# Performance work log

Measured on AMD Instinct MI355X. Metric: run time of the kernel, lower is better.

The kernel has to match this reference:

```python
import jax, jax.numpy as jnp
import numpy as np

M_MODES = 12
N_PHOTONS = 6  # input_state = [1]*6 + [0]*6


def _glynn_signs(n):
    # All delta in {+1,-1}^n with delta_0 = +1 : 2^(n-1) sign vectors.
    k = np.arange(2 ** (n - 1))
    bits = (k[:, None] >> np.arange(n - 1)[None, :]) & 1  # [S, n-1]
    signs = np.concatenate([np.ones((k.size, 1)), 1.0 - 2.0 * bits], axis=1)
    parity = np.prod(signs, axis=1)  # [S]
    return jnp.asarray(signs, jnp.float32), jnp.asarray(parity, jnp.float32)


def _batched_permanent(Msub):
    # Glynn formula: perm(M) = 2^(1-n) * sum_delta prod(delta) * prod_j sum_i delta_i M_ij
    n = Msub.shape[-1]
    signs, parity = _glynn_signs(n)
    signs = signs.astype(Msub.dtype)
    # [..., S, n] row-sums under each sign vector
    rowsums = jnp.einsum('sn,...nj->...sj', signs, Msub)
    prods = jnp.prod(rowsums, axis=-1)  # [..., S]
    perm = jnp.einsum('s,...s->...', parity.astype(Msub.dtype), prods)
    return perm / (2.0 ** (n - 1))


def _feature_unitaries(x, A, B):
    # U(x) = A @ diag(exp(i x)) @ B  (phase-shifter layer between fixed interferometers)
    ph = jnp.exp(1j * x.astype(jnp.complex64))  # [N, m]
    return jnp.einsum('ab,nb,bc->nac', A, ph, B)  # [N, m, m]


def setup_inputs() -> dict:
    key = jax.random.key(0)
    k1, k2, k3, k4 = jax.random.split(key, 4)
    x1 = jax.random.normal(k1, (384, M_MODES), jnp.float32)
    x2 = jax.random.normal(k2, (384, M_MODES), jnp.float32)
    # Fixed Haar-random unitaries for the interferometer meshes
    rng = np.random.default_rng(0)
    A = np.linalg.qr(rng.normal(size=(M_MODES, M_MODES)) + 1j * rng.normal(size=(M_MODES, M_MODES)))[0]
    B = np.linalg.qr(rng.normal(size=(M_MODES, M_MODES)) + 1j * rng.normal(size=(M_MODES, M_MODES)))[0]
    return {
        'x1': x1, 'x2': x2,
        'A_re': jnp.asarray(A.real, jnp.float32), 'A_im': jnp.asarray(A.imag, jnp.float32),
        'B_re': jnp.asarray(B.real, jnp.float32), 'B_im': jnp.asarray(B.imag, jnp.float32),
    }


def reference(x1, x2, A_re, A_im, B_re, B_im):
    A = (A_re + 1j * A_im).astype(jnp.complex64)
    B = (B_re + 1j * B_im).astype(jnp.complex64)
    U1 = _feature_unitaries(x1, A, B)  # [N1, m, m]
    U2 = _feature_unitaries(x2, A, B)  # [N2, m, m]
    n = N_PHOTONS
    # W = U(x2)^dag U(x1); amplitude = perm(W[s_idx, s_idx]) with s_idx = first n modes
    # (input_state = [1]*n + [0]*(m-n), all factorials = 1)
    Wsub = jnp.einsum('jka,ikb->ijab', jnp.conj(U2[:, :, :n]), U1[:, :, :n])  # [N1,N2,n,n]
    amp = _batched_permanent(Wsub)  # [N1, N2] complex
    K = jnp.abs(amp) ** 2
    return K.astype(jnp.float32)
```

## Files before the change

### kernel.cpp

```cpp
#include <hip/hip_runtime.h>


#define NS 384
#define MM 12
#define NP 6
#define TS 16
#define SV_STRIDE 148

struct c32 { float x, y; };

__device__ __forceinline__ c32 cmul(c32 a, c32 b) {
    c32 r;
    r.x = a.x * b.x - a.y * b.y;
    r.y = a.x * b.y + a.y * b.x;
    return r;
}

__global__ void build_V_kernel(const float* __restrict__ x1,
                               const float* __restrict__ x2,
                               const float* __restrict__ Ar, const float* __restrict__ Ai,
                               const float* __restrict__ Br, const float* __restrict__ Bi,
                               float* __restrict__ V1, float* __restrict__ V2c) {
    int idx = blockIdx.x * blockDim.x + threadIdx.x;
    if (idx >= 2 * NS * NP) return;
    int half = idx / (NS * NP);
    int rem  = idx - half * (NS * NP);
    int s = rem / NP, c = rem - s * NP;
    const float* x = half ? x2 : x1;

    float tr[MM], ti[MM];
#pragma unroll
    for (int b = 0; b < MM; ++b) {
        float sv, cv;
        sincosf(x[s * MM + b], &sv, &cv);
        float br = Br[b * MM + c], bi = Bi[b * MM + c];
        tr[b] = cv * br - sv * bi;
        ti[b] = cv * bi + sv * br;
    }

    float* V = half ? V2c : V1;
    float sgn = half ? -1.f : 1.f;
#pragma unroll
    for (int a = 0; a < MM; ++a) {
        float ure = 0.f, uim = 0.f;
#pragma unroll
        for (int b = 0; b < MM; ++b) {
            float ar = Ar[a * MM + b], ai = Ai[a * MM + b];
            ure = fmaf(ar, tr[b], fmaf(-ai, ti[b], ure));
            uim = fmaf(ar, ti[b], fmaf( ai, tr[b], uim));
        }
        int off = ((s * MM + a) * NP + c) * 2;
        V[off]     = ure;
        V[off + 1] = sgn * uim;
    }
}

__global__ __launch_bounds__(256) void perm_kernel(const float* __restrict__ V1g,
                                                   const float* __restrict__ V2g,
                                                   float* __restrict__ out) {
    __shared__ __align__(16) float sV1[TS * SV_STRIDE];
    __shared__ __align__(16) float sV2[TS * SV_STRIDE];
    const int i0 = blockIdx.y * TS;
    const int j0 = blockIdx.x * TS;
    const int tid = threadIdx.x;

    for (int idx = tid; idx < 2 * TS * 36; idx += 256) {
        int which = idx >= TS * 36;
        int rem = which ? idx - TS * 36 : idx;
        int s = rem / 36, q = rem - s * 36;
        const float* src = which ? (V2g + (j0 + s) * 144) : (V1g + (i0 + s) * 144);
        float4 v = *(const float4*)(src + q * 4);
        float* dst = (which ? sV2 : sV1) + s * SV_STRIDE + q * 4;
        *(float4*)dst = v;
    }
    __syncthreads();

    const int tx = tid & 15, ty = tid >> 4;
    const float* v1 = sV1 + ty * SV_STRIDE;
    const float* v2 = sV2 + tx * SV_STRIDE;

    c32 W[NP][NP];
#pragma unroll
    for (int a = 0; a < NP; ++a)
#pragma unroll
        for (int b = 0; b < NP; ++b) { W[a][b].x = 0.f; W[a][b].y = 0.f; }

#pragma unroll
    for (int k = 0; k < MM; ++k) {
        float4 p1[3], p2[3];
#pragma unroll
        for (int q = 0; q < 3; ++q) {
            p1[q] = *(const float4*)(v1 + k * 12 + q * 4);
            p2[q] = *(const float4*)(v2 + k * 12 + q * 4);
        }
        const float* f1 = (const float*)p1;
        const float* f2 = (const float*)p2;
#pragma unroll
        for (int a = 0; a < NP; ++a) {
            float a2x = f2[2 * a], a2y = f2[2 * a + 1];
#pragma unroll
            for (int b = 0; b < NP; ++b) {
                float a1x = f1[2 * b], a1y = f1[2 * b + 1];
                W[a][b].x = fmaf(a2x, a1x, fmaf(-a2y, a1y, W[a][b].x));
                W[a][b].y = fmaf(a2x, a1y, fmaf( a2y, a1x, W[a][b].y));
            }
        }
    }

    c32 rs[NP];
#pragma unroll
    for (int b = 0; b < NP; ++b) {
        rs[b] = W[0][b];
#pragma unroll
        for (int a = 1; a < NP; ++a) { rs[b].x += W[a][b].x; rs[b].y += W[a][b].y; }
    }

    c32 acc;
    {
        c32 p = rs[0];
#pragma unroll
        for (int b = 1; b < NP; ++b) p = cmul(p, rs[b]);
        acc = p;
    }

    unsigned state = 0;
#pragma unroll
    for (int t = 1; t < 32; ++t) {
        const int bitpos = __builtin_ctz(t);
        const int r = bitpos + 1;
        float cf = ((state >> bitpos) & 1) ? 2.f : -2.f;
        state ^= (1u << bitpos);
#pragma unroll
        for (int b = 0; b < NP; ++b) {
            rs[b].x = fmaf(cf, W[r][b].x, rs[b].x);
            rs[b].y = fmaf(cf, W[r][b].y, rs[b].y);
        }
        c32 p = rs[0];
#pragma unroll
        for (int b = 1; b < NP; ++b) p = cmul(p, rs[b]);
        float par = (t & 1) ? -1.f : 1.f;
        acc.x = fmaf(par, p.x, acc.x);
        acc.y = fmaf(par, p.y, acc.y);
    }

    float K = (acc.x * acc.x + acc.y * acc.y) * (1.f / 1024.f);
    out[(i0 + ty) * NS + (j0 + tx)] = K;
}

extern "C" void kernel_launch(void* const* d_in, const int* in_sizes, int n_in,
                              void* d_out, int out_size, void* d_ws, size_t ws_size,
                              hipStream_t stream) {
    const float* x1 = (const float*)d_in[0];
    const float* x2 = (const float*)d_in[1];
    const float* Ar = (const float*)d_in[2];
    const float* Ai = (const float*)d_in[3];
    const float* Br = (const float*)d_in[4];
    const float* Bi = (const float*)d_in[5];
    float* out = (float*)d_out;

    float* V1  = (float*)d_ws;
    float* V2c = V1 + NS * MM * NP * 2;

    int total = 2 * NS * NP;
    build_V_kernel<<<(total + 255) / 256, 256, 0, stream>>>(x1, x2, Ar, Ai, Br, Bi, V1, V2c);

    dim3 grid(NS / TS, NS / TS);
    perm_kernel<<<grid, 256, 0, stream>>>(V1, V2c, out);
}
```

Baseline: 87.07 us.

## Split Gray-code permanent into four chains, tree products, halve build_V work

The permanent kernel now splits the 32-term Glynn Gray-code loop into four independent chains, one per fixed sign pattern of rows 4 and 5, each walking 8 steps. This shortens the serial dependency chain and exposes instruction-level parallelism. The 6-way complex product becomes a tree, and cmul uses fmaf. build_V now splits each thread's output rows in half and uses fast __sincosf, which gives more threads and less precision. The extra chains raise register pressure and may lower occupancy.

```diff
diff --git a/kernel.cpp b/kernel.cpp
--- a/kernel.cpp
+++ b/kernel.cpp
@@ -11,8 +11,8 @@
 
 __device__ __forceinline__ c32 cmul(c32 a, c32 b) {
     c32 r;
-    r.x = a.x * b.x - a.y * b.y;
-    r.y = a.x * b.y + a.y * b.x;
+    r.x = fmaf(a.x, b.x, -a.y * b.y);
+    r.y = fmaf(a.x, b.y,  a.y * b.x);
     return r;
 }
 
@@ -22,26 +22,29 @@
                                const float* __restrict__ Br, const float* __restrict__ Bi,
                                float* __restrict__ V1, float* __restrict__ V2c) {
     int idx = blockIdx.x * blockDim.x + threadIdx.x;
-    if (idx >= 2 * NS * NP) return;
-    int half = idx / (NS * NP);
-    int rem  = idx - half * (NS * NP);
-    int s = rem / NP, c = rem - s * NP;
+    if (idx >= 2 * NS * NP * 2) return;
+    int ah = idx & 1;
+    int rest = idx >> 1;
+    int c = rest % NP; rest /= NP;
+    int s = rest % NS;
+    int half = rest / NS;
     const float* x = half ? x2 : x1;
 
     float tr[MM], ti[MM];
 #pragma unroll
     for (int b = 0; b < MM; ++b) {
         float sv, cv;
-        sincosf(x[s * MM + b], &sv, &cv);
+        __sincosf(x[s * MM + b], &sv, &cv);
         float br = Br[b * MM + c], bi = Bi[b * MM + c];
-        tr[b] = cv * br - sv * bi;
-        ti[b] = cv * bi + sv * br;
+        tr[b] = fmaf(cv, br, -sv * bi);
+        ti[b] = fmaf(cv, bi,  sv * br);
     }
 
     float* V = half ? V2c : V1;
     float sgn = half ? -1.f : 1.f;
 #pragma unroll
-    for (int a = 0; a < MM; ++a) {
+    for (int a0 = 0; a0 < NP; ++a0) {
+        int a = ah * NP + a0;
         float ure = 0.f, uim = 0.f;
 #pragma unroll
         for (int b = 0; b < MM; ++b) {
@@ -53,6 +56,13 @@
         V[off]     = ure;
         V[off + 1] = sgn * uim;
     }
+}
+
+__device__ __forceinline__ c32 tree_prod(const c32 rs[NP]) {
+    c32 p01 = cmul(rs[0], rs[1]);
+    c32 p23 = cmul(rs[2], rs[3]);
+    c32 p45 = cmul(rs[4], rs[5]);
+    return cmul(cmul(p01, p23), p45);
 }
 
 __global__ __launch_bounds__(256) void perm_kernel(const float* __restrict__ V1g,
@@ -107,43 +117,56 @@
         }
     }
 
-    c32 rs[NP];
+    c32 base[NP];
 #pragma unroll
     for (int b = 0; b < NP; ++b) {
-        rs[b] = W[0][b];
+        base[b] = W[0][b];
 #pragma unroll
-        for (int a = 1; a < NP; ++a) { rs[b].x += W[a][b].x; rs[b].y += W[a][b].y; }
+        for (int a = 1; a < NP; ++a) { base[b].x += W[a][b].x; base[b].y += W[a][b].y; }
     }
 
-    c32 acc;
-    {
-        c32 p = rs[0];
+    c32 rs[4][NP];
 #pragma unroll
-        for (int b = 1; b < NP; ++b) p = cmul(p, rs[b]);
-        acc = p;
+    for (int b = 0; b < NP; ++b) {
+        rs[0][b] = base[b];
+        rs[1][b].x = fmaf(-2.f, W[4][b].x, base[b].x);
+        rs[1][b].y = fmaf(-2.f, W[4][b].y, base[b].y);
+        rs[2][b].x = fmaf(-2.f, W[5][b].x, base[b].x);
+        rs[2][b].y = fmaf(-2.f, W[5][b].y, base[b].y);
+        rs[3][b].x = fmaf(-2.f, W[5][b].x, rs[1][b].x);
+        rs[3][b].y = fmaf(-2.f, W[5][b].y, rs[1][b].y);
+    }
+    float accx[4], accy[4];
+#pragma unroll
+    for (int ch = 0; ch < 4; ++ch) {
+        c32 p = tree_prod(rs[ch]);
+        accx[ch] = p.x; accy[ch] = p.y;
     }
 
-    unsigned state = 0;
+    unsigned st = 0;
 #pragma unroll
-    for (int t = 1; t < 32; ++t) {
-        const int bitpos = __builtin_ctz(t);
+    for (int u = 1; u < 8; ++u) {
+        const int bitpos = __builtin_ctz(u);
         const int r = bitpos + 1;
-        float cf = ((state >> bitpos) & 1) ? 2.f : -2.f;
-        state ^= (1u << bitpos);
+        float cf = ((st >> bitpos) & 1) ? 2.f : -2.f;
+        st ^= (1u << bitpos);
+        float sgn_u = (u & 1) ? -1.f : 1.f;
 #pragma unroll
-        for (int b = 0; b < NP; ++b) {
-            rs[b].x = fmaf(cf, W[r][b].x, rs[b].x);
-            rs[b].y = fmaf(cf, W[r][b].y, rs[b].y);
+        for (int ch = 0; ch < 4; ++ch) {
+#pragma unroll
+            for (int b = 0; b < NP; ++b) {
+                rs[ch][b].x = fmaf(cf, W[r][b].x, rs[ch][b].x);
+                rs[ch][b].y = fmaf(cf, W[r][b].y, rs[ch][b].y);
+            }
+            c32 p = tree_prod(rs[ch]);
+            accx[ch] = fmaf(sgn_u, p.x, accx[ch]);
+            accy[ch] = fmaf(sgn_u, p.y, accy[ch]);
         }
-        c32 p = rs[0];
-#pragma unroll
-        for (int b = 1; b < NP; ++b) p = cmul(p, rs[b]);
-        float par = (t & 1) ? -1.f : 1.f;
-        acc.x = fmaf(par, p.x, acc.x);
-        acc.y = fmaf(par, p.y, acc.y);
     }
 
-    float K = (acc.x * acc.x + acc.y * acc.y) * (1.f / 1024.f);
+    float ax = accx[0] - accx[1] - accx[2] + accx[3];
+    float ay = accy[0] - accy[1] - accy[2] + accy[3];
+    float K = fmaf(ax, ax, ay * ay) * (1.f / 1024.f);
     out[(i0 + ty) * NS + (j0 + tx)] = K;
 }
 
@@ -161,7 +184,7 @@
     float* V1  = (float*)d_ws;
     float* V2c = V1 + NS * MM * NP * 2;
 
-    int total = 2 * NS * NP;
+    int total = 2 * NS * NP * 2;
     build_V_kernel<<<(total + 255) / 256, 256, 0, stream>>>(x1, x2, Ar, Ai, Br, Bi, V1, V2c);
 
     dim3 grid(NS / TS, NS / TS);
```

Result: faster. 80.73 us (-7.3%).
